# Performance work log

Hardware: AMD Instinct MI355X
Metric: run time of the kernel (lower is better)

Reference implementation:

```python
import jax, jax.numpy as jnp
import numpy as np
import math

D_MODEL = 1024
NHEAD = 16
NUM_CLUSTERS = 32
L, N, S = 2048, 2, 2048
LN_EPS = 1e-5


def setup_inputs() -> dict:
    key = jax.random.key(0)
    ks = jax.random.split(key, 16)
    E = D_MODEL
    s = 1.0 / math.sqrt(E)
    cq = jax.random.normal(ks[0], (NUM_CLUSTERS, E), jnp.float32)
    cq = cq / jnp.linalg.norm(cq, axis=1, keepdims=True)
    ck = jax.random.normal(ks[1], (NUM_CLUSTERS, E), jnp.float32)
    ck = ck / jnp.linalg.norm(ck, axis=1, keepdims=True)
    return {
        "query": jax.random.normal(ks[2], (L, N, E), jnp.float32),
        "key": jax.random.normal(ks[3], (S, N, E), jnp.float32),
        "value": jax.random.normal(ks[4], (S, N, E), jnp.float32),
        "Wq": jax.random.uniform(ks[5], (E, E), jnp.float32, -s, s),
        "bq": jax.random.uniform(ks[6], (E,), jnp.float32, -s, s),
        "Wk": jax.random.uniform(ks[7], (E, E), jnp.float32, -s, s),
        "bk": jax.random.uniform(ks[8], (E,), jnp.float32, -s, s),
        "Wv": jax.random.uniform(ks[9], (E, E), jnp.float32, -s, s),
        "bv": jax.random.uniform(ks[10], (E,), jnp.float32, -s, s),
        "Wo": jax.random.uniform(ks[11], (E, E), jnp.float32, -s, s),
        "bo": jax.random.uniform(ks[12], (E,), jnp.float32, -s, s),
        "centroids_q": cq,
        "centroids_k": ck,
        "ln_gamma": jnp.ones((E,), jnp.float32),
        "ln_beta": jnp.zeros((E,), jnp.float32),
    }


def _assign(x, centroids):
    # spherical k-means assignment: argmax cosine similarity
    xn = x / jnp.clip(jnp.linalg.norm(x, axis=-1, keepdims=True), 1e-12)
    return jnp.argmax(xn @ centroids.T, axis=-1)


def reference(query, key, value, Wq, bq, Wk, bk, Wv, bv, Wo, bo,
              centroids_q, centroids_k, ln_gamma, ln_beta):
    Lq, Nb, E = query.shape
    Sk = key.shape[0]
    H, dh = NHEAD, E // NHEAD

    Q = query @ Wq.T + bq            # [L,N,E]
    K = key @ Wk.T + bk              # [S,N,E]
    V = value @ Wv.T + bv            # [S,N,E]

    Qb = jnp.transpose(Q, (1, 0, 2))  # [N,L,E]
    Kb = jnp.transpose(K, (1, 0, 2))  # [N,S,E]
    Vb = jnp.transpose(V, (1, 0, 2))  # [N,S,E]

    q_clusters = _assign(Qb, centroids_q)  # [N,L] int
    k_clusters = _assign(Kb, centroids_k)  # [N,S] int
    # bipartite cluster-equality mask, broadcast over heads
    mask = q_clusters[:, :, None] == k_clusters[:, None, :]  # [N,L,S]

    Qh = Qb.reshape(Nb, Lq, H, dh)
    Kh = Kb.reshape(Nb, Sk, H, dh)
    Vh = Vb.reshape(Nb, Sk, H, dh)

    scores = jnp.einsum('nlhd,nshd->nhls', Qh, Kh) / math.sqrt(dh)
    scores = jnp.where(mask[:, None, :, :], scores, -jnp.inf)
    attn = jax.nn.softmax(scores, axis=-1)  # dropout = identity (eval)

    ctx = jnp.einsum('nhls,nshd->nlhd', attn, Vh).reshape(Nb, Lq, E)
    out = ctx @ Wo.T + bo                     # [N,L,E]
    out = jnp.transpose(out, (1, 0, 2))       # [L,N,E]

    res = query + out
    mu = jnp.mean(res, axis=-1, keepdims=True)
    var = jnp.mean(jnp.square(res - mu), axis=-1, keepdims=True)
    return (res - mu) / jnp.sqrt(var + LN_EPS) * ln_gamma + ln_beta
```

## Files before the change

kernel.cpp:

```cpp
#include <hip/hip_runtime.h>
#include <stdint.h>

#define L_SEQ 2048
#define S_SEQ 2048
#define NB 2
#define EMB 1024
#define NH 16
#define DH 64
#define NC 32
#define MROWS 4096

typedef __bf16 bf16x8 __attribute__((ext_vector_type(8)));
typedef float f32x4 __attribute__((ext_vector_type(4)));

__device__ __forceinline__ float bf2f(unsigned short u) {
  return __builtin_bit_cast(float, (uint32_t)u << 16);
}
__device__ __forceinline__ unsigned short f2bf(float f) {
  uint32_t u = __builtin_bit_cast(uint32_t, f);
  return (unsigned short)((u + 0x7FFFu + ((u >> 16) & 1u)) >> 16);
}

#if defined(__has_builtin) && __has_builtin(__builtin_amdgcn_global_load_lds)
#define GLOAD_LDS(gp, lp)                                            \
  __builtin_amdgcn_global_load_lds(                                  \
      (const __attribute__((address_space(1))) void*)(gp),           \
      (__attribute__((address_space(3))) void*)(lp), 16, 0, 0)
#else
#define GLOAD_LDS(gp, lp) do { *(uint4*)(lp) = *(const uint4*)(gp); } while (0)
#endif

__global__ void __launch_bounds__(256) conv_f2bf_kernel(
    const float* __restrict__ srcW, unsigned short* __restrict__ dstW, int nW8,
    const float* __restrict__ srcX, unsigned short* __restrict__ dstX, int nX8)
{
  int id = blockIdx.x * 256 + threadIdx.x;
  const float* src; unsigned short* dst; int i;
  if (id < nW8) { src = srcW; dst = dstW; i = id; }
  else { i = id - nW8; if (i >= nX8) return; src = srcX; dst = dstX; }
  const float4* s = (const float4*)src + (size_t)i * 2;
  float4 a0 = s[0], a1 = s[1];
  uint4 u;
  u.x = (uint32_t)f2bf(a0.x) | ((uint32_t)f2bf(a0.y) << 16);
  u.y = (uint32_t)f2bf(a0.z) | ((uint32_t)f2bf(a0.w) << 16);
  u.z = (uint32_t)f2bf(a1.x) | ((uint32_t)f2bf(a1.y) << 16);
  u.w = (uint32_t)f2bf(a1.z) | ((uint32_t)f2bf(a1.w) << 16);
  ((uint4*)dst)[i] = u;
}

__global__ void __launch_bounds__(256) gemm_bt_mfma(
    const unsigned short* __restrict__ A, const unsigned short* __restrict__ B,
    const float* __restrict__ bias,
    float* __restrict__ outF, unsigned short* __restrict__ outB)
{
  __shared__ __align__(16) unsigned short As[128][32];
  __shared__ __align__(16) unsigned short Bs[128][32];
  const int K = EMB;
  int tid = threadIdx.x;
  int m0 = blockIdx.y * 128, n0 = blockIdx.x * 128;
  int wave = tid >> 6, lane = tid & 63;
  int wm = (wave >> 1) * 64, wn = (wave & 1) * 64;

  f32x4 zero = {0.f, 0.f, 0.f, 0.f};
  f32x4 acc[4][4];
#pragma unroll
  for (int mi = 0; mi < 4; mi++)
#pragma unroll
    for (int ni = 0; ni < 4; ni++) acc[mi][ni] = zero;

  int fr = lane & 15, fk = (lane >> 4) * 8;

  for (int k0 = 0; k0 < K; k0 += 32) {
    __syncthreads();
#pragma unroll
    for (int it = 0; it < 2; it++) {
      int ch = tid + it * 256;
      int row = ch >> 2, kk = (ch & 3) * 8;
      GLOAD_LDS(A + (size_t)(m0 + row) * K + k0 + kk, &As[row][kk]);
      GLOAD_LDS(B + (size_t)(n0 + row) * K + k0 + kk, &Bs[row][kk]);
    }
    __syncthreads();
    bf16x8 af[4], bfr[4];
#pragma unroll
    for (int i = 0; i < 4; i++) af[i] = *(const bf16x8*)(&As[wm + i * 16 + fr][fk]);
#pragma unroll
    for (int i = 0; i < 4; i++) bfr[i] = *(const bf16x8*)(&Bs[wn + i * 16 + fr][fk]);
#pragma unroll
    for (int mi = 0; mi < 4; mi++)
#pragma unroll
      for (int ni = 0; ni < 4; ni++)
        acc[mi][ni] = __builtin_amdgcn_mfma_f32_16x16x32_bf16(af[mi], bfr[ni], acc[mi][ni], 0, 0, 0);
  }

#pragma unroll
  for (int ni = 0; ni < 4; ni++) {
    int col = n0 + wn + ni * 16 + (lane & 15);
    float bv = bias[col];
#pragma unroll
    for (int mi = 0; mi < 4; mi++) {
#pragma unroll
      for (int r = 0; r < 4; r++) {
        int row = m0 + wm + mi * 16 + (lane >> 4) * 4 + r;
        float v = acc[mi][ni][r] + bv;
        if (outF) outF[(size_t)row * EMB + col] = v;
        else outB[(size_t)row * EMB + col] = f2bf(v);
      }
    }
  }
}

__global__ void __launch_bounds__(256) prep_partial_kernel(
    const float* __restrict__ Wq_, const float* __restrict__ cq_,
    const float* __restrict__ Wk_, const float* __restrict__ ck_,
    double* __restrict__ partQ, double* __restrict__ partK)
{
  const float* W; const float* cent; double* part;
  if (blockIdx.z == 0) { W = Wq_; cent = cq_; part = partQ; }
  else                 { W = Wk_; cent = ck_; part = partK; }
  int tid = threadIdx.x;
  int k = (blockIdx.y << 6) | (tid & 63);
  int cbase = __builtin_amdgcn_readfirstlane(tid >> 6) * 8;
  int e0 = blockIdx.x << 6;

  double acc[8];
#pragma unroll
  for (int j = 0; j < 8; j++) acc[j] = 0.0;

#pragma unroll 2
  for (int e = 0; e < 64; e++) {
    double w = (double)W[(size_t)(e0 + e) * EMB + k];
#pragma unroll
    for (int j = 0; j < 8; j++)
      acc[j] += w * (double)cent[(size_t)(cbase + j) * EMB + e0 + e];
  }
#pragma unroll
  for (int j = 0; j < 8; j++)
    part[((size_t)blockIdx.x * NC + cbase + j) * EMB + k] = acc[j];
}

__global__ void __launch_bounds__(256) prep_reduce_kernel(
    const double* __restrict__ partQ, const double* __restrict__ partK,
    double* __restrict__ WcTq, double* __restrict__ WcTk)
{
  int id = blockIdx.x * 256 + threadIdx.x;
  const double* part; double* WcT; int local;
  if (id < NC * EMB) { part = partQ; WcT = WcTq; local = id; }
  else               { part = partK; WcT = WcTk; local = id - NC * EMB; }
  int c = local >> 10, k = local & 1023;
  double s = 0.0;
  for (int es = 0; es < 16; es++)
    s += part[((size_t)es * NC + c) * EMB + k];
  WcT[(size_t)k * NC + c] = s;
}

__global__ void __launch_bounds__(256) prep_bd_kernel(
    const float* __restrict__ bq_, const float* __restrict__ cq_,
    const float* __restrict__ bk_, const float* __restrict__ ck_,
    double* __restrict__ bdq, double* __restrict__ bdk)
{
  const float* bias; const float* cent; double* bd;
  if (blockIdx.x == 0) { bias = bq_; cent = cq_; bd = bdq; }
  else                 { bias = bk_; cent = ck_; bd = bdk; }
  int tid = threadIdx.x;
  int c = tid & 31, g = tid >> 5;
  __shared__ double red[8][32];
  double s2 = 0.0;
  for (int e = g * 128; e < (g + 1) * 128; e++)
    s2 += (double)bias[e] * (double)cent[(size_t)c * EMB + e];
  red[g][c] = s2;
  __syncthreads();
  if (tid < 32) {
    double t = 0.0;
#pragma unroll
    for (int gg = 0; gg < 8; gg++) t += red[gg][tid];
    bd[tid] = t;
  }
}

__global__ void __launch_bounds__(256) assign2_kernel(
    const float* __restrict__ Xq, const double* __restrict__ WcTq, const double* __restrict__ bdq,
    int* __restrict__ qcl, int* __restrict__ qcnt,
    const float* __restrict__ Xk, const double* __restrict__ WcTk, const double* __restrict__ bdk,
    int* __restrict__ kcl, int* __restrict__ kcnt)
{
  const float* X; const double* WcT; const double* bd; int* cluster; int* count;
  if (blockIdx.y == 0) { X = Xq; WcT = WcTq; bd = bdq; cluster = qcl; count = qcnt; }
  else                 { X = Xk; WcT = WcTk; bd = bdk; cluster = kcl; count = kcnt; }

  int r0 = blockIdx.x * 32;
  int tid = threadIdx.x;
  int c = tid & 31, g = tid >> 5;
  int g4 = g * 4;

  __shared__ __align__(16) double Ws[64][32];
  __shared__ __align__(16) float  Xs[32][64];

  double a[4][4];
#pragma unroll
  for (int rr = 0; rr < 4; rr++)
#pragma unroll
    for (int j = 0; j < 4; j++) a[rr][j] = 0.0;

  for (int k0 = 0; k0 < EMB; k0 += 64) {
    __syncthreads();
#pragma unroll
    for (int it = 0; it < 8; it++) {
      int idx = it * 256 + tid;
      ((double*)Ws)[idx] = WcT[(size_t)k0 * NC + idx];
    }
#pragma unroll
    for (int it = 0; it < 2; it++) {
      int idx = it * 256 + tid;
      int r = idx >> 4, kp = (idx & 15) * 4;
      *(float4*)(&Xs[r][kp]) = *(const float4*)(X + (size_t)(r0 + r) * EMB + k0 + kp);
    }
    __syncthreads();
#pragma unroll
    for (int ks = 0; ks < 64; ks += 8) {
      double w0 = Ws[ks + 0][c], w1 = Ws[ks + 1][c];
      double w2 = Ws[ks + 2][c], w3 = Ws[ks + 3][c];
      double w4 = Ws[ks + 4][c], w5 = Ws[ks + 5][c];
      double w6 = Ws[ks + 6][c], w7 = Ws[ks + 7][c];
#pragma unroll
      for (int rr = 0; rr < 4; rr++) {
        float4 xa = *(const float4*)(&Xs[g4 + rr][ks]);
        float4 xb = *(const float4*)(&Xs[g4 + rr][ks + 4]);
        a[rr][0] += (double)xa.x * w0; a[rr][1] += (double)xa.y * w1;
        a[rr][2] += (double)xa.z * w2; a[rr][3] += (double)xa.w * w3;
        a[rr][0] += (double)xb.x * w4; a[rr][1] += (double)xb.y * w5;
        a[rr][2] += (double)xb.z * w6; a[rr][3] += (double)xb.w * w7;
      }
    }
  }

  double bdc = bd[c];
#pragma unroll
  for (int rr = 0; rr < 4; rr++) {
    double dot = ((a[rr][0] + a[rr][1]) + (a[rr][2] + a[rr][3])) + bdc;
    double bv = dot; int bi = c;
#pragma unroll
    for (int off = 1; off < 32; off <<= 1) {
      double ov = __shfl_xor(bv, off, 64);
      int oi = __shfl_xor(bi, off, 64);
      if (ov > bv || (ov == bv && oi < bi)) { bv = ov; bi = oi; }
    }
    if (c == 0) {
      int row = r0 + g4 + rr;
      cluster[row] = bi;
      atomicAdd(&count[(row & 1) * NC + bi], 1);
    }
  }
}

__global__ void scan_kernel(const int* __restrict__ qcount, const int* __restrict__ kcount,
                            int* __restrict__ qoff, int* __restrict__ koff)
{
  int tid = threadIdx.x;
  if (tid < 2) {
    int run = 0;
    for (int c = 0; c < NC; c++) { qoff[tid * NC + c] = run; run += qcount[tid * NC + c]; }
  } else if (tid < 4) {
    int n = tid - 2, run = 0;
    for (int c = 0; c < NC; c++) { koff[n * NC + c] = run; run += kcount[n * NC + c]; }
  }
}

__global__ void __launch_bounds__(256) scatter_kernel(
    const int* __restrict__ q_cluster, const int* __restrict__ k_cluster,
    const int* __restrict__ qoff, const int* __restrict__ koff,
    int* __restrict__ qfill, int* __restrict__ kfill,
    int* __restrict__ qlist, int* __restrict__ klist)
{
  int id = blockIdx.x * 256 + threadIdx.x;
  if (id < MROWS) {
    int row = id, n = row & 1, l = row >> 1, c = q_cluster[row];
    int pos = atomicAdd(&qfill[n * NC + c], 1);
    qlist[n * L_SEQ + qoff[n * NC + c] + pos] = l;
  } else {
    int row = id - MROWS, n = row & 1, s = row >> 1, c = k_cluster[row];
    int pos = atomicAdd(&kfill[n * NC + c], 1);
    klist[n * S_SEQ + koff[n * NC + c] + pos] = s;
  }
}

__global__ void __launch_bounds__(256) attn_bucket(
    const unsigned short* __restrict__ Qb, const unsigned short* __restrict__ Kb,
    const unsigned short* __restrict__ Vb,
    const int* __restrict__ qcount, const int* __restrict__ qoff, const int* __restrict__ qlist,
    const int* __restrict__ kcount, const int* __restrict__ koff, const int* __restrict__ klist,
    unsigned short* __restrict__ ctx)
{
  int c = blockIdx.x, h = blockIdx.y, n = blockIdx.z;
  int Sc = kcount[n * NC + c], k0base = koff[n * NC + c];
  int Lc = qcount[n * NC + c], q0 = qoff[n * NC + c];
  int tid = threadIdx.x, wave = tid >> 6, lane = tid & 63;
  int lg = lane >> 4, lq = lane & 15;

  __shared__ __align__(16) unsigned short Ks[64][64];
  __shared__ __align__(16) unsigned short Vts[64][64];
  __shared__ __align__(16) unsigned short Pts[4][16][64];
  __shared__ int rb[64];

  if (Sc == 0) {
    for (int qi = wave; qi < Lc; qi += 4) {
      int l = qlist[n * L_SEQ + q0 + qi];
      ctx[((size_t)(n * L_SEQ + l)) * EMB + h * DH + lane] = 0;
    }
    return;
  }

  const int* kl = klist + n * S_SEQ + k0base;
  const int* ql = qlist + n * L_SEQ + q0;
  f32x4 zero = {0.f, 0.f, 0.f, 0.f};

  for (int qb = 0; qb < Lc; qb += 64) {
    int qq = qb + wave * 16 + lq;
    int qqc = qq < Lc ? qq : Lc - 1;
    int lrow = ql[qqc];
    const unsigned short* qp = Qb + ((size_t)(lrow * NB + n)) * EMB + h * DH;
    bf16x8 qf0 = *(const bf16x8*)(qp + lg * 8);
    bf16x8 qf1 = *(const bf16x8*)(qp + 32 + lg * 8);

    f32x4 acc[4];
#pragma unroll
    for (int di = 0; di < 4; di++) acc[di] = zero;
    float m = -3.0e38f, lsum = 0.f;

    for (int kc = 0; kc < Sc; kc += 64) {
      __syncthreads();
      if (tid < 64) {
        int jj = kc + tid; if (jj >= Sc) jj = Sc - 1;
        rb[tid] = (kl[jj] * NB + n) * EMB + h * DH;
      }
      __syncthreads();
#pragma unroll
      for (int it = 0; it < 2; it++) {
        int p = it * 256 + tid;
        {
          int row = p >> 3, seg = p & 7;
          uint4 u = *(const uint4*)(Kb + rb[row] + seg * 8);
          *(uint4*)(&Ks[row][(seg * 8) ^ ((row & 7) << 3)]) = u;
        }
        {
          int d = p & 63, kg = p >> 6;
          unsigned short v0 = Vb[rb[kg * 8 + 0] + d], v1 = Vb[rb[kg * 8 + 1] + d];
          unsigned short v2 = Vb[rb[kg * 8 + 2] + d], v3 = Vb[rb[kg * 8 + 3] + d];
          unsigned short v4 = Vb[rb[kg * 8 + 4] + d], v5 = Vb[rb[kg * 8 + 5] + d];
          unsigned short v6 = Vb[rb[kg * 8 + 6] + d], v7 = Vb[rb[kg * 8 + 7] + d];
          uint4 u;
          u.x = (uint32_t)v0 | ((uint32_t)v1 << 16);
          u.y = (uint32_t)v2 | ((uint32_t)v3 << 16);
          u.z = (uint32_t)v4 | ((uint32_t)v5 << 16);
          u.w = (uint32_t)v6 | ((uint32_t)v7 << 16);
          *(uint4*)(&Vts[d][(kg * 8) ^ ((d & 7) << 3)]) = u;
        }
      }
      __syncthreads();

      f32x4 st[4];
#pragma unroll
      for (int ni = 0; ni < 4; ni++) st[ni] = zero;
#pragma unroll
      for (int ni = 0; ni < 4; ni++) {
        int row = ni * 16 + lq;
        bf16x8 kf0 = *(const bf16x8*)(&Ks[row][(lg * 8) ^ ((row & 7) << 3)]);
        bf16x8 kf1 = *(const bf16x8*)(&Ks[row][(32 + lg * 8) ^ ((row & 7) << 3)]);
        st[ni] = __builtin_amdgcn_mfma_f32_16x16x32_bf16(kf0, qf0, st[ni], 0, 0, 0);
        st[ni] = __builtin_amdgcn_mfma_f32_16x16x32_bf16(kf1, qf1, st[ni], 0, 0, 0);
      }

      int lim = Sc - kc;
      float cm = -3.0e38f;
#pragma unroll
      for (int ni = 0; ni < 4; ni++) {
        st[ni] = st[ni] * 0.125f;
#pragma unroll
        for (int r = 0; r < 4; r++) cm = fmaxf(cm, st[ni][r]);
      }
      cm = fmaxf(cm, __shfl_xor(cm, 16, 64));
      cm = fmaxf(cm, __shfl_xor(cm, 32, 64));
      float mn = fmaxf(m, cm);
      float fac = __expf(m - mn);
      m = mn;
      lsum *= fac;
#pragma unroll
      for (int di = 0; di < 4; di++) acc[di] = acc[di] * fac;

#pragma unroll
      for (int ni = 0; ni < 4; ni++) {
        int kloc = ni * 16 + lg * 4;
        float p0 = (kloc + 0 < lim) ? __expf(st[ni][0] - mn) : 0.f;
        float p1 = (kloc + 1 < lim) ? __expf(st[ni][1] - mn) : 0.f;
        float p2 = (kloc + 2 < lim) ? __expf(st[ni][2] - mn) : 0.f;
        float p3 = (kloc + 3 < lim) ? __expf(st[ni][3] - mn) : 0.f;
        unsigned short b0 = f2bf(p0), b1 = f2bf(p1), b2 = f2bf(p2), b3 = f2bf(p3);
        lsum += bf2f(b0) + bf2f(b1) + bf2f(b2) + bf2f(b3);
        ushort4 u4; u4.x = b0; u4.y = b1; u4.z = b2; u4.w = b3;
        *(ushort4*)(&Pts[wave][lq][kloc ^ ((lq & 7) << 3)]) = u4;
      }

#pragma unroll
      for (int ks = 0; ks < 2; ks++) {
        bf16x8 pf = *(const bf16x8*)(&Pts[wave][lq][(ks * 32 + lg * 8) ^ ((lq & 7) << 3)]);
#pragma unroll
        for (int di = 0; di < 4; di++) {
          int row = di * 16 + lq;
          bf16x8 vf = *(const bf16x8*)(&Vts[row][(ks * 32 + lg * 8) ^ ((row & 7) << 3)]);
          acc[di] = __builtin_amdgcn_mfma_f32_16x16x32_bf16(vf, pf, acc[di], 0, 0, 0);
        }
      }
    }

    lsum += __shfl_xor(lsum, 16, 64);
    lsum += __shfl_xor(lsum, 32, 64);
    float rinv = 1.f / lsum;
    if (qq < Lc) {
      unsigned short* op = ctx + ((size_t)(n * L_SEQ + lrow)) * EMB + h * DH;
#pragma unroll
      for (int di = 0; di < 4; di++) {
        ushort4 o;
        o.x = f2bf(acc[di][0] * rinv);
        o.y = f2bf(acc[di][1] * rinv);
        o.z = f2bf(acc[di][2] * rinv);
        o.w = f2bf(acc[di][3] * rinv);
        *(ushort4*)(op + di * 16 + lg * 4) = o;
      }
    }
  }
}

__global__ void __launch_bounds__(256) ln_kernel(
    const float* __restrict__ proj, const float* __restrict__ query,
    const float* __restrict__ gamma, const float* __restrict__ beta,
    float* __restrict__ out)
{
  int r = blockIdx.x;
  int l = r >> 1, n = r & 1;
  int tid = threadIdx.x, wave = tid >> 6, lane = tid & 63;
  float4 p = *(const float4*)(proj + ((size_t)(n * L_SEQ + l)) * EMB + tid * 4);
  float4 qu = *(const float4*)(query + (size_t)r * EMB + tid * 4);
  float res[4] = { p.x + qu.x, p.y + qu.y, p.z + qu.z, p.w + qu.w };
  float s1 = res[0] + res[1] + res[2] + res[3];
  float s2 = res[0] * res[0] + res[1] * res[1] + res[2] * res[2] + res[3] * res[3];
#pragma unroll
  for (int off = 32; off; off >>= 1) {
    s1 += __shfl_xor(s1, off, 64);
    s2 += __shfl_xor(s2, off, 64);
  }
  __shared__ float a1[4], a2[4];
  if (lane == 0) { a1[wave] = s1; a2[wave] = s2; }
  __syncthreads();
  float t1 = a1[0] + a1[1] + a1[2] + a1[3];
  float t2 = a2[0] + a2[1] + a2[2] + a2[3];
  float mu = t1 * (1.f / EMB);
  float var = fmaxf(t2 * (1.f / EMB) - mu * mu, 0.f);
  float rstd = 1.f / sqrtf(var + 1e-5f);
  float4 gu = *(const float4*)(gamma + tid * 4);
  float4 bu = *(const float4*)(beta + tid * 4);
  float4 o;
  o.x = (res[0] - mu) * rstd * gu.x + bu.x;
  o.y = (res[1] - mu) * rstd * gu.y + bu.y;
  o.z = (res[2] - mu) * rstd * gu.z + bu.z;
  o.w = (res[3] - mu) * rstd * gu.w + bu.w;
  *(float4*)(out + (size_t)r * EMB + tid * 4) = o;
}

extern "C" void kernel_launch(void* const* d_in, const int* in_sizes, int n_in,
                              void* d_out, int out_size, void* d_ws, size_t ws_size,
                              hipStream_t stream) {
  const float* query = (const float*)d_in[0];
  const float* key   = (const float*)d_in[1];
  const float* value = (const float*)d_in[2];
  const float* Wq = (const float*)d_in[3];
  const float* bq = (const float*)d_in[4];
  const float* Wk = (const float*)d_in[5];
  const float* bk = (const float*)d_in[6];
  const float* Wv = (const float*)d_in[7];
  const float* bv = (const float*)d_in[8];
  const float* Wo = (const float*)d_in[9];
  const float* bo = (const float*)d_in[10];
  const float* cq = (const float*)d_in[11];
  const float* ck = (const float*)d_in[12];
  const float* gamma = (const float*)d_in[13];
  const float* beta  = (const float*)d_in[14];
  float* out = (float*)d_out;

  const size_t MB_EL = (size_t)MROWS * EMB;

  int* q_cluster = (int*)d_ws;
  int* k_cluster = q_cluster + MROWS;
  int* qcount = k_cluster + MROWS;
  int* kcount = qcount + 64;
  int* qoff   = kcount + 64;
  int* koff   = qoff + 64;
  int* qfill  = koff + 64;
  int* kfill  = qfill + 64;
  int* qlist  = kfill + 64;
  int* klist  = qlist + MROWS;
  double* Wcq = (double*)(klist + MROWS);
  double* Wck = Wcq + (size_t)NC * EMB;
  double* bdq = Wck + (size_t)NC * EMB;
  double* bdk = bdq + NC;
  unsigned short* Qb  = (unsigned short*)(bdk + NC);
  unsigned short* Kb  = Qb + MB_EL;
  unsigned short* Vb  = Kb + MB_EL;
  unsigned short* ctx = Vb + MB_EL;
  unsigned short* wbf = ctx + MB_EL;
  unsigned short* xbf = ctx;
  float* proj = (float*)Qb;
  double* partQ = (double*)Qb;
  double* partK = partQ + (size_t)16 * NC * EMB;

  const int W8 = (EMB * EMB) / 8;
  const int X8 = (int)(MB_EL / 8);
  const int CVT_BLK = (W8 + X8 + 255) / 256;

  hipMemsetAsync(qcount, 0, 6 * 64 * sizeof(int), stream);

  prep_partial_kernel<<<dim3(16, 16, 2), 256, 0, stream>>>(Wq, cq, Wk, ck, partQ, partK);
  prep_reduce_kernel<<<(2 * NC * EMB) / 256, 256, 0, stream>>>(partQ, partK, Wcq, Wck);
  prep_bd_kernel<<<2, 256, 0, stream>>>(bq, cq, bk, ck, bdq, bdk);

  dim3 gg(EMB / 128, MROWS / 128);
  conv_f2bf_kernel<<<CVT_BLK, 256, 0, stream>>>(Wq, wbf, W8, query, xbf, X8);
  gemm_bt_mfma<<<gg, 256, 0, stream>>>(xbf, wbf, bq, nullptr, Qb);

  conv_f2bf_kernel<<<CVT_BLK, 256, 0, stream>>>(Wk, wbf, W8, key, xbf, X8);
  gemm_bt_mfma<<<gg, 256, 0, stream>>>(xbf, wbf, bk, nullptr, Kb);

  conv_f2bf_kernel<<<CVT_BLK, 256, 0, stream>>>(Wv, wbf, W8, value, xbf, X8);
  gemm_bt_mfma<<<gg, 256, 0, stream>>>(xbf, wbf, bv, nullptr, Vb);

  assign2_kernel<<<dim3(MROWS / 32, 2), 256, 0, stream>>>(
      query, Wcq, bdq, q_cluster, qcount,
      key,   Wck, bdk, k_cluster, kcount);

  scan_kernel<<<1, 64, 0, stream>>>(qcount, kcount, qoff, koff);
  scatter_kernel<<<(2 * MROWS) / 256, 256, 0, stream>>>(q_cluster, k_cluster, qoff, koff,
                                                        qfill, kfill, qlist, klist);
  attn_bucket<<<dim3(NC, NH, NB), 256, 0, stream>>>(Qb, Kb, Vb, qcount, qoff, qlist,
                                                    kcount, koff, klist, ctx);

  conv_f2bf_kernel<<<(W8 + 255) / 256, 256, 0, stream>>>(Wo, wbf, W8, nullptr, nullptr, 0);
  gemm_bt_mfma<<<gg, 256, 0, stream>>>(ctx, wbf, bo, proj, nullptr);
  ln_kernel<<<MROWS, 256, 0, stream>>>(proj, query, gamma, beta, out);
}
```

Measured before the change: 357.6 us.

## Fuse activation bf16 conversion into a batched QKV GEMM launch

The Q, K and V projections become one launch with a z=3 grid. Each block now reads fp32 activations straight from query, key or value and converts them to bf16 in registers before storing to LDS. This removes three separate activation-conversion passes, their intermediate buffer traffic and several kernel launches. The four weight conversions are merged into two launches that fill a contiguous QKV weight buffer and the Wo buffer. In exchange, A-tile loads become synchronous register loads with conversion work inside the GEMM loop, instead of direct global-to-LDS copies.

After: 331.8 us. 7.2% less time.

```diff
diff --git a/kernel.cpp b/kernel.cpp
--- a/kernel.cpp
+++ b/kernel.cpp
@@ -31,13 +31,13 @@
 #endif
 
 __global__ void __launch_bounds__(256) conv_f2bf_kernel(
-    const float* __restrict__ srcW, unsigned short* __restrict__ dstW, int nW8,
-    const float* __restrict__ srcX, unsigned short* __restrict__ dstX, int nX8)
+    const float* __restrict__ src1, unsigned short* __restrict__ dst1, int n1,
+    const float* __restrict__ src2, unsigned short* __restrict__ dst2, int n2)
 {
   int id = blockIdx.x * 256 + threadIdx.x;
   const float* src; unsigned short* dst; int i;
-  if (id < nW8) { src = srcW; dst = dstW; i = id; }
-  else { i = id - nW8; if (i >= nX8) return; src = srcX; dst = dstX; }
+  if (id < n1) { src = src1; dst = dst1; i = id; }
+  else { i = id - n1; if (i >= n2) return; src = src2; dst = dst2; }
   const float4* s = (const float4*)src + (size_t)i * 2;
   float4 a0 = s[0], a1 = s[1];
   uint4 u;
@@ -48,11 +48,18 @@
   ((uint4*)dst)[i] = u;
 }
 
-__global__ void __launch_bounds__(256) gemm_bt_mfma(
-    const unsigned short* __restrict__ A, const unsigned short* __restrict__ B,
-    const float* __restrict__ bias,
-    float* __restrict__ outF, unsigned short* __restrict__ outB)
-{
+__global__ void __launch_bounds__(256) gemm_qkv_mfma(
+    const float* __restrict__ Aq, const float* __restrict__ Ak, const float* __restrict__ Av,
+    const unsigned short* __restrict__ Wall,
+    const float* __restrict__ bq_, const float* __restrict__ bk_, const float* __restrict__ bv_,
+    unsigned short* __restrict__ Qb, unsigned short* __restrict__ Kb, unsigned short* __restrict__ Vb)
+{
+  int z = blockIdx.z;
+  const float* A = (z == 0) ? Aq : (z == 1) ? Ak : Av;
+  const unsigned short* B = Wall + (size_t)z * EMB * EMB;
+  const float* bias = (z == 0) ? bq_ : (z == 1) ? bk_ : bv_;
+  unsigned short* outB = (z == 0) ? Qb : (z == 1) ? Kb : Vb;
+
   __shared__ __align__(16) unsigned short As[128][32];
   __shared__ __align__(16) unsigned short Bs[128][32];
   const int K = EMB;
@@ -76,7 +83,16 @@
     for (int it = 0; it < 2; it++) {
       int ch = tid + it * 256;
       int row = ch >> 2, kk = (ch & 3) * 8;
-      GLOAD_LDS(A + (size_t)(m0 + row) * K + k0 + kk, &As[row][kk]);
+      {
+        const float* ap = A + (size_t)(m0 + row) * K + k0 + kk;
+        float4 a0 = *(const float4*)ap, a1 = *(const float4*)(ap + 4);
+        uint4 u;
+        u.x = (uint32_t)f2bf(a0.x) | ((uint32_t)f2bf(a0.y) << 16);
+        u.y = (uint32_t)f2bf(a0.z) | ((uint32_t)f2bf(a0.w) << 16);
+        u.z = (uint32_t)f2bf(a1.x) | ((uint32_t)f2bf(a1.y) << 16);
+        u.w = (uint32_t)f2bf(a1.z) | ((uint32_t)f2bf(a1.w) << 16);
+        *(uint4*)(&As[row][kk]) = u;
+      }
       GLOAD_LDS(B + (size_t)(n0 + row) * K + k0 + kk, &Bs[row][kk]);
     }
     __syncthreads();
@@ -101,9 +117,66 @@
 #pragma unroll
       for (int r = 0; r < 4; r++) {
         int row = m0 + wm + mi * 16 + (lane >> 4) * 4 + r;
-        float v = acc[mi][ni][r] + bv;
-        if (outF) outF[(size_t)row * EMB + col] = v;
-        else outB[(size_t)row * EMB + col] = f2bf(v);
+        outB[(size_t)row * EMB + col] = f2bf(acc[mi][ni][r] + bv);
+      }
+    }
+  }
+}
+
+__global__ void __launch_bounds__(256) gemm_bt_mfma(
+    const unsigned short* __restrict__ A, const unsigned short* __restrict__ B,
+    const float* __restrict__ bias,
+    float* __restrict__ outF)
+{
+  __shared__ __align__(16) unsigned short As[128][32];
+  __shared__ __align__(16) unsigned short Bs[128][32];
+  const int K = EMB;
+  int tid = threadIdx.x;
+  int m0 = blockIdx.y * 128, n0 = blockIdx.x * 128;
+  int wave = tid >> 6, lane = tid & 63;
+  int wm = (wave >> 1) * 64, wn = (wave & 1) * 64;
+
+  f32x4 zero = {0.f, 0.f, 0.f, 0.f};
+  f32x4 acc[4][4];
+#pragma unroll
+  for (int mi = 0; mi < 4; mi++)
+#pragma unroll
+    for (int ni = 0; ni < 4; ni++) acc[mi][ni] = zero;
+
+  int fr = lane & 15, fk = (lane >> 4) * 8;
+
+  for (int k0 = 0; k0 < K; k0 += 32) {
+    __syncthreads();
+#pragma unroll
+    for (int it = 0; it < 2; it++) {
+      int ch = tid + it * 256;
+      int row = ch >> 2, kk = (ch & 3) * 8;
+      GLOAD_LDS(A + (size_t)(m0 + row) * K + k0 + kk, &As[row][kk]);
+      GLOAD_LDS(B + (size_t)(n0 + row) * K + k0 + kk, &Bs[row][kk]);
+    }
+    __syncthreads();
+    bf16x8 af[4], bfr[4];
+#pragma unroll
+    for (int i = 0; i < 4; i++) af[i] = *(const bf16x8*)(&As[wm + i * 16 + fr][fk]);
+#pragma unroll
+    for (int i = 0; i < 4; i++) bfr[i] = *(const bf16x8*)(&Bs[wn + i * 16 + fr][fk]);
+#pragma unroll
+    for (int mi = 0; mi < 4; mi++)
+#pragma unroll
+      for (int ni = 0; ni < 4; ni++)
+        acc[mi][ni] = __builtin_amdgcn_mfma_f32_16x16x32_bf16(af[mi], bfr[ni], acc[mi][ni], 0, 0, 0);
+  }
+
+#pragma unroll
+  for (int ni = 0; ni < 4; ni++) {
+    int col = n0 + wn + ni * 16 + (lane & 15);
+    float bv = bias[col];
+#pragma unroll
+    for (int mi = 0; mi < 4; mi++) {
+#pragma unroll
+      for (int r = 0; r < 4; r++) {
+        int row = m0 + wm + mi * 16 + (lane >> 4) * 4 + r;
+        outF[(size_t)row * EMB + col] = acc[mi][ni][r] + bv;
       }
     }
   }
@@ -506,14 +579,12 @@
   unsigned short* Vb  = Kb + MB_EL;
   unsigned short* ctx = Vb + MB_EL;
   unsigned short* wbf = ctx + MB_EL;
-  unsigned short* xbf = ctx;
+  unsigned short* wqkv = ctx;
   float* proj = (float*)Qb;
   double* partQ = (double*)Qb;
   double* partK = partQ + (size_t)16 * NC * EMB;
 
   const int W8 = (EMB * EMB) / 8;
-  const int X8 = (int)(MB_EL / 8);
-  const int CVT_BLK = (W8 + X8 + 255) / 256;
 
   hipMemsetAsync(qcount, 0, 6 * 64 * sizeof(int), stream);
 
@@ -521,15 +592,13 @@
   prep_reduce_kernel<<<(2 * NC * EMB) / 256, 256, 0, stream>>>(partQ, partK, Wcq, Wck);
   prep_bd_kernel<<<2, 256, 0, stream>>>(bq, cq, bk, ck, bdq, bdk);
 
-  dim3 gg(EMB / 128, MROWS / 128);
-  conv_f2bf_kernel<<<CVT_BLK, 256, 0, stream>>>(Wq, wbf, W8, query, xbf, X8);
-  gemm_bt_mfma<<<gg, 256, 0, stream>>>(xbf, wbf, bq, nullptr, Qb);
-
-  conv_f2bf_kernel<<<CVT_BLK, 256, 0, stream>>>(Wk, wbf, W8, key, xbf, X8);
-  gemm_bt_mfma<<<gg, 256, 0, stream>>>(xbf, wbf, bk, nullptr, Kb);
-
-  conv_f2bf_kernel<<<CVT_BLK, 256, 0, stream>>>(Wv, wbf, W8, value, xbf, X8);
-  gemm_bt_mfma<<<gg, 256, 0, stream>>>(xbf, wbf, bv, nullptr, Vb);
+  conv_f2bf_kernel<<<(2 * W8 + 255) / 256, 256, 0, stream>>>(
+      Wq, wqkv, W8, Wk, wqkv + (size_t)EMB * EMB, W8);
+  conv_f2bf_kernel<<<(2 * W8 + 255) / 256, 256, 0, stream>>>(
+      Wv, wqkv + (size_t)2 * EMB * EMB, W8, Wo, wbf, W8);
+
+  dim3 gq(EMB / 128, MROWS / 128, 3);
+  gemm_qkv_mfma<<<gq, 256, 0, stream>>>(query, key, value, wqkv, bq, bk, bv, Qb, Kb, Vb);
 
   assign2_kernel<<<dim3(MROWS / 32, 2), 256, 0, stream>>>(
       query, Wcq, bdq, q_cluster, qcount,
@@ -541,7 +610,7 @@
   attn_bucket<<<dim3(NC, NH, NB), 256, 0, stream>>>(Qb, Kb, Vb, qcount, qoff, qlist,
                                                     kcount, koff, klist, ctx);
 
-  conv_f2bf_kernel<<<(W8 + 255) / 256, 256, 0, stream>>>(Wo, wbf, W8, nullptr, nullptr, 0);
-  gemm_bt_mfma<<<gg, 256, 0, stream>>>(ctx, wbf, bo, proj, nullptr);
+  dim3 gg(EMB / 128, MROWS / 128);
+  gemm_bt_mfma<<<gg, 256, 0, stream>>>(ctx, wbf, bo, proj);
   ln_kernel<<<MROWS, 256, 0, stream>>>(proj, query, gamma, beta, out);
 }
```
